# Performance work log

Measured on AMD Instinct MI355X. Metric: run time of the kernel, lower is better.

The kernel has to match this reference:

```python
import jax, jax.numpy as jnp
import numpy as np

N_OBJ, P, M, D = 8, 65536, 32, 128


def setup_inputs() -> dict:
    key = jax.random.key(0)
    k1, k2, k3 = jax.random.split(key, 3)
    net_out = jax.random.normal(k1, (N_OBJ * P, D), dtype=jnp.float32)
    # cumulative end offsets per object; last entry (unused by the loop) repeats N_total
    pt_offset = jnp.concatenate([
        jnp.arange(1, N_OBJ + 1, dtype=jnp.int32) * P,
        jnp.array([N_OBJ * P], dtype=jnp.int32),
    ])
    mask_pts = jax.random.randint(k2, (N_OBJ, M, P), 0, 2, dtype=jnp.int32)
    mask_embs = jax.random.normal(k3, (N_OBJ * M, D), dtype=jnp.float32)
    logit_scale = jnp.ones((1,), dtype=jnp.float32)
    return {
        "net_out": net_out,
        "pt_offset": pt_offset,
        "mask_embs": mask_embs,
        "mask_pts": mask_pts,
        "logit_scale": logit_scale,
    }


def reference(net_out, pt_offset, mask_embs, mask_pts, logit_scale):
    # Uniform segments: object o owns points [o*P, (o+1)*P), matching pt_offset.
    n_obj, n_masks, n_pts = mask_pts.shape
    d = net_out.shape[1]
    x = net_out[: n_obj * n_pts].reshape(n_obj, n_pts, d)          # [O,P,D]
    emb = jnp.nan_to_num(
        mask_embs.reshape(n_obj, n_masks, d), nan=0.0, posinf=0.0, neginf=0.0
    )                                                               # [O,M,D]
    m = mask_pts.astype(net_out.dtype)                              # [O,M,P]

    # sum_p mask * ||x_p - e||^2 = sum_p m*||x_p||^2 + cnt*||e||^2 - 2 e . (sum_p m x_p)
    cnt = jnp.sum(m, axis=-1)                                       # [O,M]
    xsq = jnp.sum(x * x, axis=-1)                                   # [O,P]
    t1 = jnp.einsum("omp,op->om", m, xsq)                          # [O,M]
    t2 = cnt * jnp.sum(emb * emb, axis=-1)                          # [O,M]
    mx = jnp.einsum("omp,opd->omd", m, x)                          # [O,M,D]
    t3 = 2.0 * jnp.sum(emb * mx, axis=-1)                           # [O,M]

    sum_sq = jnp.sum(t1 + t2 - t3)
    total_points = jnp.sum(cnt)
    # torch: sum over masks of MSE(masked_pts, label)*n_pts, divided by total points
    # MSE*n_pts = sum_sq_per_mask / D; empty masks contribute 0 to both terms.
    return jnp.where(total_points > 0, sum_sq / (d * total_points), 0.0)
```

## Files before the change

kernel.cpp:

```cpp
#include <hip/hip_runtime.h>
#include <math.h>

#define NOBJ 8
#define NP   65536
#define NM   32
#define ND   128
#define CHUNKS 64
#define PTS_WG 1024
#define PTS_WAVE 256

__launch_bounds__(256, 2)
__global__ void distill_main(const float* __restrict__ net,
                             const float* __restrict__ embs,
                             const int* __restrict__ mask,
                             float* __restrict__ ws) {
  __shared__ float T[8 * 16 * ND];
  __shared__ float esq[NM];
  __shared__ int   Wlds[4 * PTS_WAVE];
  __shared__ float red[4][4];

  const int tid  = threadIdx.x;
  const int wave = tid >> 6;
  const int lane = tid & 63;
  const int o     = blockIdx.x >> 6;
  const int chunk = blockIdx.x & (CHUNKS - 1);

  const float* EB = embs + (size_t)o * NM * ND;

  if (tid < NM) {
    float a = 0.f;
    const float* e = EB + (size_t)tid * ND;
    for (int d_ = 0; d_ < ND; ++d_) {
      float v = e[d_];
      if (!isfinite(v)) v = 0.f;
      a += v * v;
    }
    esq[tid] = a;
  }

  for (int j = 0; j < 64; ++j) {
    int idx = j * 256 + tid;
    int d_ = idx & (ND - 1);
    int n  = (idx >> 7) & 15;
    int g  = idx >> 11;
    float acc = 0.f;
#pragma unroll
    for (int b = 0; b < 4; ++b) {
      float e = EB[(size_t)(g * 4 + b) * ND + d_];
      if (!isfinite(e)) e = 0.f;
      acc += ((n >> b) & 1) ? e : 0.f;
    }
    T[idx] = acc;
  }
  __syncthreads();

  const int p0 = chunk * PTS_WG + wave * PTS_WAVE;
  const int* mp = mask + (size_t)o * NM * NP + p0 + 4 * lane;
  int W0 = 0, W1 = 0, W2 = 0, W3 = 0;
  float pB = 0.f, TPl = 0.f;
  int4 v[8], u[8];
#pragma unroll
  for (int j = 0; j < 8; ++j) v[j] = *(const int4*)(mp + (size_t)j * NP);
#pragma unroll
  for (int b = 0; b < 4; ++b) {
    if (b < 3) {
#pragma unroll
      for (int j = 0; j < 8; ++j)
        u[j] = *(const int4*)(mp + (size_t)((b + 1) * 8 + j) * NP);
    }
#pragma unroll
    for (int j = 0; j < 8; ++j) {
      const int m = b * 8 + j;
      int b0 = (v[j].x != 0), b1 = (v[j].y != 0), b2 = (v[j].z != 0), b3 = (v[j].w != 0);
      W0 |= b0 << m; W1 |= b1 << m; W2 |= b2 << m; W3 |= b3 << m;
      float c = (float)(b0 + b1 + b2 + b3);
      TPl += c;
      pB  += esq[m] * c;
    }
    if (b < 3) {
#pragma unroll
      for (int j = 0; j < 8; ++j) v[j] = u[j];
    }
  }
  *(int4*)&Wlds[wave * PTS_WAVE + 4 * lane] = make_int4(W0, W1, W2, W3);
  __syncthreads();

  const float* xo = net + ((size_t)o * NP + p0) * ND;
  const int half = lane >> 5;
  const int dl   = (lane & 31) * 4;
  const int base = wave * PTS_WAVE;
  float accA = 0.f, accC = 0.f;

  auto comp = [&](const float4 X, const int W) {
    accA += (float)__popc(W) * (X.x * X.x + X.y * X.y + X.z * X.z + X.w * X.w);
    float s0 = 0.f, s1 = 0.f, s2 = 0.f, s3 = 0.f;
#pragma unroll
    for (int g = 0; g < 8; ++g) {
      int n = (W >> (g * 4)) & 15;
      const float4 t = *(const float4*)&T[(g * 16 + n) * ND + dl];
      s0 += t.x; s1 += t.y; s2 += t.z; s3 += t.w;
    }
    accC += s0 * X.x + s1 * X.y + s2 * X.z + s3 * X.w;
  };

  float4 Xa0 = *(const float4*)(xo + (size_t)(0 + half) * ND + dl);
  float4 Xa1 = *(const float4*)(xo + (size_t)(2 + half) * ND + dl);
  float4 Xb0 = *(const float4*)(xo + (size_t)(4 + half) * ND + dl);
  float4 Xb1 = *(const float4*)(xo + (size_t)(6 + half) * ND + dl);
  int Wq0 = Wlds[base + 0 + half], Wq1 = Wlds[base + 2 + half];
  int Wq2 = Wlds[base + 4 + half], Wq3 = Wlds[base + 6 + half];

  for (int i = 0; i < PTS_WAVE; i += 8) {
    int pf = i + 8;
    pf = (pf < PTS_WAVE) ? pf : 0;
    float4 Ta0 = *(const float4*)(xo + (size_t)(pf + 0 + half) * ND + dl);
    float4 Ta1 = *(const float4*)(xo + (size_t)(pf + 2 + half) * ND + dl);
    float4 Tb0 = *(const float4*)(xo + (size_t)(pf + 4 + half) * ND + dl);
    float4 Tb1 = *(const float4*)(xo + (size_t)(pf + 6 + half) * ND + dl);
    int Tw0 = Wlds[base + pf + 0 + half], Tw1 = Wlds[base + pf + 2 + half];
    int Tw2 = Wlds[base + pf + 4 + half], Tw3 = Wlds[base + pf + 6 + half];

    comp(Xa0, Wq0);
    comp(Xa1, Wq1);
    comp(Xb0, Wq2);
    comp(Xb1, Wq3);

    Xa0 = Ta0; Xa1 = Ta1; Xb0 = Tb0; Xb1 = Tb1;
    Wq0 = Tw0; Wq1 = Tw1; Wq2 = Tw2; Wq3 = Tw3;
  }

#pragma unroll
  for (int off = 32; off >= 1; off >>= 1) {
    accA += __shfl_xor(accA, off, 64);
    accC += __shfl_xor(accC, off, 64);
    pB   += __shfl_xor(pB,   off, 64);
    TPl  += __shfl_xor(TPl,  off, 64);
  }
  if (lane == 0) {
    red[wave][0] = accA; red[wave][1] = pB;
    red[wave][2] = accC; red[wave][3] = TPl;
  }
  __syncthreads();
  if (tid == 0) {
    float A = 0.f, B = 0.f, C = 0.f, TP = 0.f;
    for (int w = 0; w < 4; ++w) {
      A += red[w][0]; B += red[w][1]; C += red[w][2]; TP += red[w][3];
    }
    atomicAdd(&ws[0], A);
    atomicAdd(&ws[1], B);
    atomicAdd(&ws[2], C);
    atomicAdd(&ws[3], TP);
  }
}

__global__ void distill_final(const float* __restrict__ ws, float* __restrict__ out) {
  float A = ws[0], B = ws[1], C = ws[2], TP = ws[3];
  out[0] = (TP > 0.f) ? (A + B - 2.f * C) / ((float)ND * TP) : 0.f;
}

extern "C" void kernel_launch(void* const* d_in, const int* in_sizes, int n_in,
                              void* d_out, int out_size, void* d_ws, size_t ws_size,
                              hipStream_t stream) {
  const float* net  = (const float*)d_in[0];
  const float* embs = (const float*)d_in[2];
  const int*   mask = (const int*)d_in[3];
  float* ws = (float*)d_ws;

  hipMemsetAsync(d_ws, 0, 4 * sizeof(float), stream);
  distill_main<<<NOBJ * CHUNKS, 256, 0, stream>>>(net, embs, mask, ws);
  distill_final<<<1, 1, 0, stream>>>(ws, (float*)d_out);
}
```

Baseline: 426.0 us.

## Pack subset-sum embedding table as bf16 in LDS and raise occupancy

Stores the precomputed 16-way subset sums of mask embeddings as packed bf16 pairs instead of fp32. This halves the LDS footprint and the LDS read traffic in the inner accumulation loop. With the smaller table, the work-group chunk shrinks to 512 points and launch bounds allow 4 blocks per CU, aiming for more occupancy and better latency hiding. The trade-off is bf16 rounding of the embedding subset sums, which adds error to the cross term of the loss.

```diff
diff --git a/kernel.cpp b/kernel.cpp
--- a/kernel.cpp
+++ b/kernel.cpp
@@ -5,16 +5,21 @@
 #define NP   65536
 #define NM   32
 #define ND   128
-#define CHUNKS 64
-#define PTS_WG 1024
-#define PTS_WAVE 256
+#define PTS_WG   512
+#define PTS_WAVE 128
+#define CHUNKS   (NP / PTS_WG)
 
-__launch_bounds__(256, 2)
+__device__ __forceinline__ unsigned f2bf(float f) {
+  unsigned u = __float_as_uint(f);
+  return (u + 0x7FFFu + ((u >> 16) & 1u)) >> 16;
+}
+
+__launch_bounds__(256, 4)
 __global__ void distill_main(const float* __restrict__ net,
                              const float* __restrict__ embs,
                              const int* __restrict__ mask,
                              float* __restrict__ ws) {
-  __shared__ float T[8 * 16 * ND];
+  __shared__ unsigned Tu[8 * 16 * 64];
   __shared__ float esq[NM];
   __shared__ int   Wlds[4 * PTS_WAVE];
   __shared__ float red[4][4];
@@ -22,7 +27,7 @@
   const int tid  = threadIdx.x;
   const int wave = tid >> 6;
   const int lane = tid & 63;
-  const int o     = blockIdx.x >> 6;
+  const int o     = blockIdx.x >> 7;
   const int chunk = blockIdx.x & (CHUNKS - 1);
 
   const float* EB = embs + (size_t)o * NM * ND;
@@ -38,42 +43,46 @@
     esq[tid] = a;
   }
 
-  for (int j = 0; j < 64; ++j) {
-    int idx = j * 256 + tid;
-    int d_ = idx & (ND - 1);
-    int n  = (idx >> 7) & 15;
-    int g  = idx >> 11;
-    float acc = 0.f;
+  for (int it = 0; it < 32; ++it) {
+    int idx = it * 256 + tid;
+    int s = idx & 63, n = (idx >> 6) & 15, g = idx >> 10;
+    int c = s & 31, j = s >> 5;
+    int d0 = 2 * (2 * c + j) * 2;
+    d0 = (2 * c + j) * 2;
+    float a0 = 0.f, a1 = 0.f;
 #pragma unroll
     for (int b = 0; b < 4; ++b) {
-      float e = EB[(size_t)(g * 4 + b) * ND + d_];
-      if (!isfinite(e)) e = 0.f;
-      acc += ((n >> b) & 1) ? e : 0.f;
+      float e0 = EB[(size_t)(g * 4 + b) * ND + d0];
+      float e1 = EB[(size_t)(g * 4 + b) * ND + d0 + 1];
+      if (!isfinite(e0)) e0 = 0.f;
+      if (!isfinite(e1)) e1 = 0.f;
+      float take = (float)((n >> b) & 1);
+      a0 += take * e0;
+      a1 += take * e1;
     }
-    T[idx] = acc;
+    Tu[idx] = f2bf(a0) | (f2bf(a1) << 16);
   }
-  __syncthreads();
 
   const int p0 = chunk * PTS_WG + wave * PTS_WAVE;
-  const int* mp = mask + (size_t)o * NM * NP + p0 + 4 * lane;
-  int W0 = 0, W1 = 0, W2 = 0, W3 = 0;
+  const int* mp = mask + (size_t)o * NM * NP + p0 + 2 * lane;
+  int WA = 0, WB = 0;
   float pB = 0.f, TPl = 0.f;
-  int4 v[8], u[8];
+  int2 v[8], u[8];
 #pragma unroll
-  for (int j = 0; j < 8; ++j) v[j] = *(const int4*)(mp + (size_t)j * NP);
+  for (int j = 0; j < 8; ++j) v[j] = *(const int2*)(mp + (size_t)j * NP);
 #pragma unroll
   for (int b = 0; b < 4; ++b) {
     if (b < 3) {
 #pragma unroll
       for (int j = 0; j < 8; ++j)
-        u[j] = *(const int4*)(mp + (size_t)((b + 1) * 8 + j) * NP);
+        u[j] = *(const int2*)(mp + (size_t)((b + 1) * 8 + j) * NP);
     }
 #pragma unroll
     for (int j = 0; j < 8; ++j) {
       const int m = b * 8 + j;
-      int b0 = (v[j].x != 0), b1 = (v[j].y != 0), b2 = (v[j].z != 0), b3 = (v[j].w != 0);
-      W0 |= b0 << m; W1 |= b1 << m; W2 |= b2 << m; W3 |= b3 << m;
-      float c = (float)(b0 + b1 + b2 + b3);
+      int bx = (v[j].x != 0), by = (v[j].y != 0);
+      WA |= bx << m; WB |= by << m;
+      float c = (float)(bx + by);
       TPl += c;
       pB  += esq[m] * c;
     }
@@ -82,12 +91,13 @@
       for (int j = 0; j < 8; ++j) v[j] = u[j];
     }
   }
-  *(int4*)&Wlds[wave * PTS_WAVE + 4 * lane] = make_int4(W0, W1, W2, W3);
+  *(int2*)&Wlds[wave * PTS_WAVE + 2 * lane] = make_int2(WA, WB);
   __syncthreads();
 
   const float* xo = net + ((size_t)o * NP + p0) * ND;
   const int half = lane >> 5;
-  const int dl   = (lane & 31) * 4;
+  const int c    = lane & 31;
+  const int dl   = c * 4;
   const int base = wave * PTS_WAVE;
   float accA = 0.f, accC = 0.f;
 
@@ -97,8 +107,13 @@
 #pragma unroll
     for (int g = 0; g < 8; ++g) {
       int n = (W >> (g * 4)) & 15;
-      const float4 t = *(const float4*)&T[(g * 16 + n) * ND + dl];
-      s0 += t.x; s1 += t.y; s2 += t.z; s3 += t.w;
+      int ix = g * 1024 + n * 64 + c;
+      unsigned uA = Tu[ix];
+      unsigned uB = Tu[ix + 32];
+      s0 += __uint_as_float(uA << 16);
+      s1 += __uint_as_float(uA & 0xffff0000u);
+      s2 += __uint_as_float(uB << 16);
+      s3 += __uint_as_float(uB & 0xffff0000u);
     }
     accC += s0 * X.x + s1 * X.y + s2 * X.z + s3 * X.w;
   };
```

Result: slower. 454.4 us (+6.7%).
